# Kernel tuning notes

Hardware: AMD Instinct MI355X
Metric: run time of the kernel (lower is better)

The kernel has to match this reference:

```python
import jax, jax.numpy as jnp
import numpy as np

SEQ, D_IN, D_OUT = 8192, 768, 64


def setup_inputs() -> dict:
    key = jax.random.key(0)
    kx, kq, kk, kv = jax.random.split(key, 4)
    scale = 1.0 / np.sqrt(D_IN)
    return {
        "x": jax.random.normal(kx, (SEQ, D_IN), dtype=jnp.float32),
        # torch Linear weight layout: [d_out, d_in]
        "W_Q": jax.random.uniform(kq, (D_OUT, D_IN), dtype=jnp.float32, minval=-scale, maxval=scale),
        "W_K": jax.random.uniform(kk, (D_OUT, D_IN), dtype=jnp.float32, minval=-scale, maxval=scale),
        "W_V": jax.random.uniform(kv, (D_OUT, D_IN), dtype=jnp.float32, minval=-scale, maxval=scale),
    }


def reference(x, W_Q, W_K, W_V):
    # q,k,v: [seq, d_out]
    q = x @ W_Q.T
    k = x @ W_K.T
    v = x @ W_V.T
    scores = (q @ k.T) / jnp.sqrt(jnp.asarray(k.shape[-1], x.dtype))  # [seq, seq]
    attn = jax.nn.softmax(scores, axis=-1)
    return attn @ v  # [seq, d_out]
```

## Files before the change

### kernel.cpp

```cpp
#include <hip/hip_runtime.h>
#include <hip/hip_bf16.h>
#include <math.h>

#define SEQ 8192
#define DIN 768
#define DOUT 64
#define QSCALE 0.1803368801111214f

typedef __attribute__((ext_vector_type(8))) short short8;
typedef __attribute__((ext_vector_type(4))) short short4v;
typedef __attribute__((ext_vector_type(4))) float floatx4;
typedef __attribute__((ext_vector_type(2))) unsigned int uint2v;

__device__ __forceinline__ void gload16(const void* g, void* l) {
    __builtin_amdgcn_global_load_lds(
        (const __attribute__((address_space(1))) unsigned int*)g,
        (__attribute__((address_space(3))) unsigned int*)l, 16, 0, 0);
}

__device__ __forceinline__ unsigned pack2(float a, float b) {
    __hip_bfloat162 h = __float22bfloat162_rn(make_float2(a, b));
    return *(unsigned*)&h;
}

__device__ __forceinline__ unsigned short bfbits(float f) {
    __hip_bfloat16 h = __float2bfloat16(f);
    return *(unsigned short*)&h;
}

__device__ __forceinline__ float exp2r(float x) {
#if __has_builtin(__builtin_amdgcn_exp2f)
    return __builtin_amdgcn_exp2f(x);
#else
    float r; asm("v_exp_f32 %0, %1" : "=v"(r) : "v"(x)); return r;
#endif
}

__device__ __forceinline__ floatx4 mfma16(short4v a, short4v b, floatx4 c) {
#if __has_builtin(__builtin_amdgcn_mfma_f32_16x16x16bf16_1k)
    return __builtin_amdgcn_mfma_f32_16x16x16bf16_1k(a, b, c, 0, 0, 0);
#else
    asm("v_mfma_f32_16x16x16_bf16 %0, %1, %2, %0" : "+v"(c) : "v"(a), "v"(b));
    return c;
#endif
}

#define BAR()       asm volatile("s_barrier" ::: "memory")
#define WAIT_VM4()  asm volatile("s_waitcnt vmcnt(4)" ::: "memory")
#define WAIT_VM0()  asm volatile("s_waitcnt vmcnt(0)" ::: "memory")

__global__ __launch_bounds__(512) void qkv_mfma(
    const float* __restrict__ x,
    const float* __restrict__ Wq, const float* __restrict__ Wk,
    const float* __restrict__ Wv,
    unsigned short* __restrict__ qbf, unsigned short* __restrict__ kbf,
    unsigned short* __restrict__ vtbf)
{
    __shared__ __align__(16) unsigned char xs[2][32 * 128];
    __shared__ __align__(16) unsigned char wsm[2][192 * 128];

    const int t = threadIdx.x;
    const int l = t & 63;
    const int wid = t >> 6;
    const int h = wid & 1;
    const int ntb = (wid >> 1) * 3;
    const int g = l >> 4;
    const int q4 = l & 15;
    const int row0 = blockIdx.x * 32;

    const int wrow0 = (t >> 3) * 3;
    const int wc8   = t & 7;
    const int xrow = t >> 4;
    const int xc4  = t & 15;

    float4 wreg[3][2];
    float4 xA, xB, x0;

#define WLOAD(k0)                                                             \
    {                                                                         \
        _Pragma("unroll")                                                     \
        for (int rr = 0; rr < 3; ++rr) {                                      \
            const int row = wrow0 + rr;                                       \
            const float* wp = (row < 64)  ? &Wq[(size_t)row * DIN]            \
                           : (row < 128) ? &Wk[(size_t)(row - 64) * DIN]      \
                                         : &Wv[(size_t)(row - 128) * DIN];    \
            wreg[rr][0] = *(const float4*)&wp[(k0) + wc8 * 8];                \
            wreg[rr][1] = *(const float4*)&wp[(k0) + wc8 * 8 + 4];            \
        }                                                                     \
    }
#define WWRITE(buf)                                                           \
    {                                                                         \
        _Pragma("unroll")                                                     \
        for (int rr = 0; rr < 3; ++rr) {                                      \
            const int row = wrow0 + rr;                                       \
            uint4 v;                                                          \
            v.x = pack2(wreg[rr][0].x, wreg[rr][0].y);                        \
            v.y = pack2(wreg[rr][0].z, wreg[rr][0].w);                        \
            v.z = pack2(wreg[rr][1].x, wreg[rr][1].y);                        \
            v.w = pack2(wreg[rr][1].z, wreg[rr][1].w);                        \
            *(uint4*)&wsm[buf][row * 128 + ((wc8 ^ (row & 7)) << 4)] = v;     \
        }                                                                     \
    }
#define XLOAD(dst, k0)                                                        \
    dst = *(const float4*)&x[(size_t)(row0 + xrow) * DIN + (k0) + xc4 * 4];
#define XWRITE(buf, src)                                                      \
    {                                                                         \
        uint2 v2;                                                             \
        v2.x = pack2(src.x, src.y);                                           \
        v2.y = pack2(src.z, src.w);                                           \
        const int half = xc4 & 1, slq = xc4 >> 1;                             \
        *(uint2*)&xs[buf][xrow * 128 + ((slq ^ (xrow & 7)) << 4) + half * 8] = v2; \
    }

    floatx4 acc[3];
#pragma unroll
    for (int i = 0; i < 3; ++i) acc[i] = (floatx4){0.f, 0.f, 0.f, 0.f};

    WLOAD(0)
    XLOAD(x0, 0)
    XLOAD(xA, 64)
    XLOAD(xB, 128)
    WWRITE(0)
    XWRITE(0, x0)
    WLOAD(64)
    __syncthreads();

#pragma unroll
    for (int kc = 0; kc < 12; ++kc) {
        const int cur = kc & 1;

        __builtin_amdgcn_s_setprio(1);
#pragma unroll
        for (int ks = 0; ks < 2; ++ks) {
            const int sl = g + 4 * ks;
            const int Rx = h * 16 + q4;
            const short8 a = *(const short8*)&xs[cur][Rx * 128 + ((sl ^ (Rx & 7)) << 4)];
#pragma unroll
            for (int j = 0; j < 3; ++j) {
                const int Rw = (ntb + j) * 16 + q4;
                const short8 b = *(const short8*)&wsm[cur][Rw * 128 + ((sl ^ (Rw & 7)) << 4)];
                acc[j] = __builtin_amdgcn_mfma_f32_16x16x32_bf16(a, b, acc[j], 0, 0, 0);
            }
        }
        __builtin_amdgcn_s_setprio(0);

        if (kc + 1 < 12) {
            WWRITE(cur ^ 1)
            if ((kc + 1) & 1) { XWRITE(cur ^ 1, xA) } else { XWRITE(cur ^ 1, xB) }
            if (kc + 2 < 12) WLOAD((kc + 2) * 64)
            if (kc + 3 < 12) {
                if ((kc + 3) & 1) { XLOAD(xA, (kc + 3) * 64) }
                else             { XLOAD(xB, (kc + 3) * 64) }
            }
        }
        __syncthreads();
    }

    const int rb = row0 + h * 16 + (g << 2);
#pragma unroll
    for (int j = 0; j < 3; ++j) {
        const int nt = ntb + j;
#pragma unroll
        for (int r = 0; r < 4; ++r) {
            const float v = acc[j][r];
            const int R = rb + r;
            if (nt < 4) {
                qbf[(size_t)R * 64 + nt * 16 + q4] = bfbits(v * QSCALE);
            } else if (nt < 8) {
                kbf[(size_t)R * 64 + (nt - 4) * 16 + q4] = bfbits(v);
            } else {
                vtbf[(size_t)((nt - 8) * 16 + q4) * SEQ + R] = bfbits(v);
            }
        }
    }
#undef WLOAD
#undef WWRITE
#undef XLOAD
#undef XWRITE
}

__global__ __launch_bounds__(256, 4) void flash_mfma(
    const unsigned short* __restrict__ qbf,
    const unsigned short* __restrict__ kbf,
    const unsigned short* __restrict__ vtbf,
    float* __restrict__ opart,
    float* __restrict__ ml,
    int nsplit, int direct)
{
    __shared__ __align__(16) unsigned char lds[32768];
    unsigned char* lkb = lds;
    unsigned char* lvb = lds + 16384;

    const int t = threadIdx.x;
    const int l = t & 63;
    const int g = l >> 4;
    const int q4 = l & 15;
    const int wid = t >> 6;
    const int row0 = blockIdx.x * 128;
    const int split = blockIdx.y;
    const int chunk = SEQ / nsplit;
    const int kbeg = split * chunk;
    const int NT = chunk / 64;

#define ISSUE_KV(buf, kt)                                                     \
    {                                                                         \
        const int Rr = l >> 3;                                                \
        const int sl = (l & 7) ^ Rr;                                          \
        _Pragma("unroll")                                                     \
        for (int ss = 0; ss < 2; ++ss) {                                      \
            const int s = wid * 2 + ss;                                       \
            const int R = 8 * s + Rr;                                         \
            gload16(&kbf[(size_t)((kt) + R) * 64 + sl * 8],                   \
                    lkb + (buf) * 8192 + s * 1024);                           \
            gload16(&vtbf[(size_t)R * SEQ + (kt) + sl * 8],                   \
                    lvb + (buf) * 8192 + s * 1024);                           \
        }                                                                     \
    }

    short8 qf[2][2];
#pragma unroll
    for (int qt = 0; qt < 2; ++qt)
#pragma unroll
        for (int ks = 0; ks < 2; ++ks)
            qf[qt][ks] = *(const short8*)&qbf[
                (size_t)(row0 + wid * 32 + qt * 16 + q4) * 64 + (g + 4 * ks) * 8];

    ISSUE_KV(0, kbeg)
    if (NT > 1) ISSUE_KV(1, kbeg + 64)

    floatx4 oacc[2][4];
#pragma unroll
    for (int i = 0; i < 2; ++i)
#pragma unroll
        for (int j = 0; j < 4; ++j) oacc[i][j] = (floatx4){0.f, 0.f, 0.f, 0.f};
    floatx4 l_acc[2] = {(floatx4){0.f, 0.f, 0.f, 0.f},
                        (floatx4){0.f, 0.f, 0.f, 0.f}};

    int cur = 0;
    for (int tt = 0; tt < NT; ++tt) {
        if (tt + 1 < NT) { WAIT_VM4(); } else { WAIT_VM0(); }
        BAR();

        const unsigned char* lk = lkb + cur * 8192;
        const unsigned char* lv = lvb + cur * 8192;

        floatx4 sacc[2][4];
#pragma unroll
        for (int i = 0; i < 2; ++i)
#pragma unroll
            for (int j = 0; j < 4; ++j) sacc[i][j] = (floatx4){0.f, 0.f, 0.f, 0.f};
        __builtin_amdgcn_s_setprio(1);
#pragma unroll
        for (int ks = 0; ks < 2; ++ks) {
            const int sl = g + 4 * ks;
#pragma unroll
            for (int nt = 0; nt < 4; ++nt) {
                const int R = nt * 16 + q4;
                const short8 kf = *(const short8*)&lk[R * 128 + ((sl ^ (R & 7)) << 4)];
                sacc[0][nt] = __builtin_amdgcn_mfma_f32_16x16x32_bf16(kf, qf[0][ks], sacc[0][nt], 0, 0, 0);
                sacc[1][nt] = __builtin_amdgcn_mfma_f32_16x16x32_bf16(kf, qf[1][ks], sacc[1][nt], 0, 0, 0);
            }
        }
        __builtin_amdgcn_s_setprio(0);

        floatx4 pv[2][4];
#pragma unroll
        for (int qt = 0; qt < 2; ++qt) {
#pragma unroll
            for (int nt = 0; nt < 4; ++nt) {
                pv[qt][nt][0] = exp2r(sacc[qt][nt][0]);
                pv[qt][nt][1] = exp2r(sacc[qt][nt][1]);
                pv[qt][nt][2] = exp2r(sacc[qt][nt][2]);
                pv[qt][nt][3] = exp2r(sacc[qt][nt][3]);
            }
            l_acc[qt] += (pv[qt][0] + pv[qt][1]) + (pv[qt][2] + pv[qt][3]);
        }

        __builtin_amdgcn_s_setprio(1);
#pragma unroll
        for (int kb = 0; kb < 4; ++kb) {
            const short4v pb0 = __builtin_bit_cast(short4v,
                (uint2v){pack2(pv[0][kb][0], pv[0][kb][1]),
                         pack2(pv[0][kb][2], pv[0][kb][3])});
            const short4v pb1 = __builtin_bit_cast(short4v,
                (uint2v){pack2(pv[1][kb][0], pv[1][kb][1]),
                         pack2(pv[1][kb][2], pv[1][kb][3])});
            const int sl = kb * 2 + (g >> 1);
#pragma unroll
            for (int dt = 0; dt < 4; ++dt) {
                const int R = dt * 16 + q4;
                const short4v a = *(const short4v*)&lv[R * 128 +
                    ((sl ^ (R & 7)) << 4) + ((g & 1) << 3)];
                oacc[0][dt] = mfma16(a, pb0, oacc[0][dt]);
                oacc[1][dt] = mfma16(a, pb1, oacc[1][dt]);
            }
        }
        __builtin_amdgcn_s_setprio(0);

        BAR();
        if (tt + 2 < NT) ISSUE_KV(cur, kbeg + (tt + 2) * 64)
        cur ^= 1;
    }

    float l_run[2];
#pragma unroll
    for (int qt = 0; qt < 2; ++qt) {
        float s = (l_acc[qt][0] + l_acc[qt][1]) + (l_acc[qt][2] + l_acc[qt][3]);
        s += __shfl_xor(s, 16);
        s += __shfl_xor(s, 32);
        l_run[qt] = s;
    }

    if (!direct && g == 0) {
#pragma unroll
        for (int qt = 0; qt < 2; ++qt) {
            const size_t mrow = (size_t)split * SEQ + row0 + wid * 32 + qt * 16 + q4;
            ml[mrow * 2 + 0] = 0.0f;
            ml[mrow * 2 + 1] = l_run[qt];
        }
    }

    float* trans = (float*)lds;
    float* outbase = direct ? opart : opart + (size_t)split * SEQ * 64;
#pragma unroll
    for (int qt = 0; qt < 2; ++qt) {
        __syncthreads();
        {
            const int r = wid * 16 + q4;
            const float sc = direct ? (1.0f / l_run[qt]) : 1.0f;
#pragma unroll
            for (int dt = 0; dt < 4; ++dt)
                *(floatx4*)&trans[r * 68 + dt * 16 + g * 4] = oacc[qt][dt] * sc;
        }
        __syncthreads();
#pragma unroll
        for (int it = 0; it < 4; ++it) {
            const int r = it * 16 + (t >> 4);
            const int qrow = row0 + ((r >> 4) << 5) + qt * 16 + (r & 15);
            const floatx4 v = *(const floatx4*)&trans[r * 68 + (t & 15) * 4];
            *(floatx4*)&outbase[(size_t)qrow * 64 + (t & 15) * 4] = v;
        }
    }
#undef ISSUE_KV
}

__global__ __launch_bounds__(256) void combine_kernel(
    const float* __restrict__ opart, const float* __restrict__ ml,
    float* __restrict__ out, int nsplit)
{
    const int i4 = blockIdx.x * 256 + threadIdx.x;
    if (i4 >= SEQ * DOUT / 4) return;
    const int row = (i4 * 4) >> 6;

    float denom = 0.f;
    floatx4 acc = (floatx4){0.f, 0.f, 0.f, 0.f};
    for (int s = 0; s < nsplit; ++s) {
        denom += ml[((size_t)s * SEQ + row) * 2 + 1];
        acc += *(const floatx4*)&opart[(size_t)s * SEQ * DOUT + i4 * 4];
    }
    acc *= (1.0f / denom);
    *(floatx4*)&out[i4 * 4] = acc;
}

extern "C" void kernel_launch(void* const* d_in, const int* in_sizes, int n_in,
                              void* d_out, int out_size, void* d_ws, size_t ws_size,
                              hipStream_t stream)
{
    const float* x  = (const float*)d_in[0];
    const float* Wq = (const float*)d_in[1];
    const float* Wk = (const float*)d_in[2];
    const float* Wv = (const float*)d_in[3];
    float* out = (float*)d_out;
    unsigned char* ws = (unsigned char*)d_ws;

    const size_t qkv_b = (size_t)SEQ * 64 * 2;
    size_t off = 0;
    unsigned short* qbf  = (unsigned short*)(ws + off); off += qkv_b;
    unsigned short* kbf  = (unsigned short*)(ws + off); off += qkv_b;
    unsigned short* vtbf = (unsigned short*)(ws + off); off += qkv_b;

    const size_t per_split = (size_t)SEQ * 64 * 4 + (size_t)SEQ * 2 * 4;
    int nsplit = 0;
    if      (ws_size >= off + 8 * per_split) nsplit = 8;
    else if (ws_size >= off + 4 * per_split) nsplit = 4;
    else if (ws_size >= off + 2 * per_split) nsplit = 2;

    qkv_mfma<<<SEQ / 32, 512, 0, stream>>>(x, Wq, Wk, Wv, qbf, kbf, vtbf);

    if (nsplit == 0) {
        flash_mfma<<<dim3(SEQ / 128, 1), 256, 0, stream>>>(
            qbf, kbf, vtbf, out, nullptr, 1, 1);
    } else {
        float* opart = (float*)(ws + off);
        float* mlp   = (float*)(ws + off + (size_t)nsplit * SEQ * 64 * 4);
        flash_mfma<<<dim3(SEQ / 128, nsplit), 256, 0, stream>>>(
            qbf, kbf, vtbf, opart, mlp, nsplit, 0);
        combine_kernel<<<(SEQ * DOUT / 4 + 255) / 256, 256, 0, stream>>>(
            opart, mlp, out, nsplit);
    }
}
```

Before: 53.54 us.

## Store split-K partial outputs in bf16 and raise split count to 16

Partial attention outputs from each key split are now written as bf16 instead of fp32, halving the workspace traffic between the flash kernel and the combine kernel. The combine kernel reads 8 bf16 values per thread and accumulates in fp32. Because each split needs less workspace, up to 16 splits are now allowed, giving more blocks per query tile for parallelism. The cost is extra rounding error in the partial sums and more combine work per output element.

New measurement: 53.14 us (median of 2 runs). Within noise of the previous version (-0.7%).

```diff
diff --git a/kernel.cpp b/kernel.cpp
--- a/kernel.cpp
+++ b/kernel.cpp
@@ -26,6 +26,11 @@
 __device__ __forceinline__ unsigned short bfbits(float f) {
     __hip_bfloat16 h = __float2bfloat16(f);
     return *(unsigned short*)&h;
+}
+
+__device__ __forceinline__ float bf2f(unsigned short u) {
+    unsigned v = ((unsigned)u) << 16;
+    return *(float*)&v;
 }
 
 __device__ __forceinline__ float exp2r(float x) {
@@ -183,7 +188,7 @@
     const unsigned short* __restrict__ qbf,
     const unsigned short* __restrict__ kbf,
     const unsigned short* __restrict__ vtbf,
-    float* __restrict__ opart,
+    void* __restrict__ opart,
     float* __restrict__ ml,
     int nsplit, int direct)
 {
@@ -320,46 +325,79 @@
         }
     }
 
-    float* trans = (float*)lds;
-    float* outbase = direct ? opart : opart + (size_t)split * SEQ * 64;
-#pragma unroll
-    for (int qt = 0; qt < 2; ++qt) {
-        __syncthreads();
-        {
-            const int r = wid * 16 + q4;
-            const float sc = direct ? (1.0f / l_run[qt]) : 1.0f;
-#pragma unroll
-            for (int dt = 0; dt < 4; ++dt)
-                *(floatx4*)&trans[r * 68 + dt * 16 + g * 4] = oacc[qt][dt] * sc;
-        }
-        __syncthreads();
-#pragma unroll
-        for (int it = 0; it < 4; ++it) {
-            const int r = it * 16 + (t >> 4);
-            const int qrow = row0 + ((r >> 4) << 5) + qt * 16 + (r & 15);
-            const floatx4 v = *(const floatx4*)&trans[r * 68 + (t & 15) * 4];
-            *(floatx4*)&outbase[(size_t)qrow * 64 + (t & 15) * 4] = v;
+    if (direct) {
+        float* trans = (float*)lds;
+        float* outbase = (float*)opart;
+#pragma unroll
+        for (int qt = 0; qt < 2; ++qt) {
+            __syncthreads();
+            {
+                const int r = wid * 16 + q4;
+                const float sc = 1.0f / l_run[qt];
+#pragma unroll
+                for (int dt = 0; dt < 4; ++dt)
+                    *(floatx4*)&trans[r * 68 + dt * 16 + g * 4] = oacc[qt][dt] * sc;
+            }
+            __syncthreads();
+#pragma unroll
+            for (int it = 0; it < 4; ++it) {
+                const int r = it * 16 + (t >> 4);
+                const int qrow = row0 + ((r >> 4) << 5) + qt * 16 + (r & 15);
+                const floatx4 v = *(const floatx4*)&trans[r * 68 + (t & 15) * 4];
+                *(floatx4*)&outbase[(size_t)qrow * 64 + (t & 15) * 4] = v;
+            }
+        }
+    } else {
+        unsigned short* transb = (unsigned short*)lds;
+        unsigned short* outb = (unsigned short*)opart + (size_t)split * SEQ * 64;
+#pragma unroll
+        for (int qt = 0; qt < 2; ++qt) {
+            __syncthreads();
+            {
+                const int r = wid * 16 + q4;
+#pragma unroll
+                for (int dt = 0; dt < 4; ++dt) {
+                    uint2 v2;
+                    v2.x = pack2(oacc[qt][dt][0], oacc[qt][dt][1]);
+                    v2.y = pack2(oacc[qt][dt][2], oacc[qt][dt][3]);
+                    *(uint2*)&transb[r * 72 + dt * 16 + g * 4] = v2;
+                }
+            }
+            __syncthreads();
+#pragma unroll
+            for (int it = 0; it < 2; ++it) {
+                const int r = it * 32 + (t >> 3);
+                const int qrow = row0 + ((r >> 4) << 5) + qt * 16 + (r & 15);
+                const short8 v = *(const short8*)&transb[r * 72 + (t & 7) * 8];
+                *(short8*)&outb[(size_t)qrow * 64 + (t & 7) * 8] = v;
+            }
         }
     }
 #undef ISSUE_KV
 }
 
 __global__ __launch_bounds__(256) void combine_kernel(
-    const float* __restrict__ opart, const float* __restrict__ ml,
+    const unsigned short* __restrict__ opart, const float* __restrict__ ml,
     float* __restrict__ out, int nsplit)
 {
-    const int i4 = blockIdx.x * 256 + threadIdx.x;
-    if (i4 >= SEQ * DOUT / 4) return;
-    const int row = (i4 * 4) >> 6;
+    const int i8 = (blockIdx.x * 256 + threadIdx.x) * 8;
+    if (i8 >= SEQ * DOUT) return;
+    const int row = i8 >> 6;
 
     float denom = 0.f;
-    floatx4 acc = (floatx4){0.f, 0.f, 0.f, 0.f};
+    float acc[8] = {0.f, 0.f, 0.f, 0.f, 0.f, 0.f, 0.f, 0.f};
     for (int s = 0; s < nsplit; ++s) {
         denom += ml[((size_t)s * SEQ + row) * 2 + 1];
-        acc += *(const floatx4*)&opart[(size_t)s * SEQ * DOUT + i4 * 4];
-    }
-    acc *= (1.0f / denom);
-    *(floatx4*)&out[i4 * 4] = acc;
+        const short8 v = *(const short8*)&opart[(size_t)s * SEQ * DOUT + i8];
+#pragma unroll
+        for (int j = 0; j < 8; ++j)
+            acc[j] += bf2f((unsigned short)v[j]);
+    }
+    const float inv = 1.0f / denom;
+    floatx4 o0 = {acc[0] * inv, acc[1] * inv, acc[2] * inv, acc[3] * inv};
+    floatx4 o1 = {acc[4] * inv, acc[5] * inv, acc[6] * inv, acc[7] * inv};
+    *(floatx4*)&out[i8] = o0;
+    *(floatx4*)&out[i8 + 4] = o1;
 }
 
 extern "C" void kernel_launch(void* const* d_in, const int* in_sizes, int n_in,
@@ -379,23 +417,24 @@
     unsigned short* kbf  = (unsigned short*)(ws + off); off += qkv_b;
     unsigned short* vtbf = (unsigned short*)(ws + off); off += qkv_b;
 
-    const size_t per_split = (size_t)SEQ * 64 * 4 + (size_t)SEQ * 2 * 4;
+    const size_t per_split = (size_t)SEQ * 64 * 2 + (size_t)SEQ * 2 * 4;
     int nsplit = 0;
-    if      (ws_size >= off + 8 * per_split) nsplit = 8;
-    else if (ws_size >= off + 4 * per_split) nsplit = 4;
-    else if (ws_size >= off + 2 * per_split) nsplit = 2;
+    if      (ws_size >= off + 16 * per_split) nsplit = 16;
+    else if (ws_size >= off + 8 * per_split)  nsplit = 8;
+    else if (ws_size >= off + 4 * per_split)  nsplit = 4;
+    else if (ws_size >= off + 2 * per_split)  nsplit = 2;
 
     qkv_mfma<<<SEQ / 32, 512, 0, stream>>>(x, Wq, Wk, Wv, qbf, kbf, vtbf);
 
     if (nsplit == 0) {
         flash_mfma<<<dim3(SEQ / 128, 1), 256, 0, stream>>>(
-            qbf, kbf, vtbf, out, nullptr, 1, 1);
+            qbf, kbf, vtbf, (void*)out, nullptr, 1, 1);
     } else {
-        float* opart = (float*)(ws + off);
-        float* mlp   = (float*)(ws + off + (size_t)nsplit * SEQ * 64 * 4);
+        unsigned short* opart = (unsigned short*)(ws + off);
+        float* mlp = (float*)(ws + off + (size_t)nsplit * SEQ * 64 * 2);
         flash_mfma<<<dim3(SEQ / 128, nsplit), 256, 0, stream>>>(
-            qbf, kbf, vtbf, opart, mlp, nsplit, 0);
-        combine_kernel<<<(SEQ * DOUT / 4 + 255) / 256, 256, 0, stream>>>(
+            qbf, kbf, vtbf, (void*)opart, mlp, nsplit, 0);
+        combine_kernel<<<SEQ * DOUT / 8 / 256, 256, 0, stream>>>(
             opart, mlp, out, nsplit);
     }
 }
```
